# Kernel tuning notes

Hardware: AMD Instinct MI355X
Metric: run time of the kernel (lower is better)

The kernel has to match this reference:

```python
import jax, jax.numpy as jnp
import numpy as np

B, S, D, E, TOPK, H = 8, 2048, 2048, 8, 2, 16
DH = D // H          # head_dim = 128
FH = D // H          # head_hidden_dim = 128 (hidden == dim, forced by linear3 shapes)
ROUTE_LEN = 2048     # x0 = x[:, :2048]


def setup_inputs() -> dict:
    key = jax.random.key(0)
    ks = jax.random.split(key, 8)
    s = 0.02
    return {
        "x": jax.random.normal(ks[0], (B, S, D), jnp.float32),
        "switch_w": jax.random.normal(ks[1], (E, D * ROUTE_LEN), jnp.float32) * s,
        "switch_b": jnp.zeros((E,), jnp.float32),
        "w1": jax.random.normal(ks[2], (E, FH, DH), jnp.float32) * s,
        "b1": jnp.zeros((E, FH), jnp.float32),
        "w2": jax.random.normal(ks[3], (E, DH, FH), jnp.float32) * s,
        "b2": jnp.zeros((E, DH), jnp.float32),
        "w3": jax.random.normal(ks[4], (D, D), jnp.float32) * s,
        "b3": jnp.zeros((D,), jnp.float32),
    }


def reference(x, switch_w, switch_b, w1, b1, w2, b2, w3, b3):
    b, s, d = x.shape
    # --- router: per batch-sample softmax over experts, top-k selection ---
    x0 = x[:, :ROUTE_LEN].reshape(b, -1)                      # [B, 2048*D]
    logits = x0 @ switch_w.T + switch_b                       # [B, E]
    probs = jax.nn.softmax(logits, axis=-1)
    gate, top_idx = jax.lax.top_k(probs, TOPK)                # [B, K]
    # --- split heads ---
    xh = x.reshape(b, s, H, DH).transpose(0, 2, 1, 3)         # [B, H, S, Dh]
    # --- per-sample gather of selected expert weights (dense grouped GEMM) ---
    w1s, b1s = w1[top_idx], b1[top_idx]                       # [B,K,F,Dh], [B,K,F]
    w2s, b2s = w2[top_idx], b2[top_idx]                       # [B,K,Dh,F], [B,K,Dh]
    h = jnp.einsum('bhsd,bkfd->bkhsf', xh, w1s) + b1s[:, :, None, None, :]
    h = jax.nn.gelu(h, approximate=False)                     # torch nn.GELU is exact
    o = jnp.einsum('bkhsf,bkdf->bkhsd', h, w2s) + b2s[:, :, None, None, :]
    # gate-weighted combine over selected experts (index_add_ sums the k copies)
    o = (o * gate[:, :, None, None, None]).sum(axis=1)        # [B, H, S, Dh]
    o = o.transpose(0, 2, 1, 3).reshape(b, s, d)              # combine heads
    out = x + o                                               # residual
    return out @ w3.T + b3                                    # linear3
```

## Files before the change

kernel.cpp:

```cpp
#include <hip/hip_runtime.h>
#include <math.h>

typedef unsigned short u16;
typedef unsigned int u32;
typedef __attribute__((ext_vector_type(8))) short short8;
typedef __attribute__((ext_vector_type(4))) float f32x4;
typedef __attribute__((ext_vector_type(4))) unsigned short ushort4v;

#define B_ 8
#define S_ 2048
#define D_ 2048
#define H_ 16
#define RLEN 4194304
#define NCHUNK 512

static __device__ __forceinline__ u16 f2bf(float f) {
    union { float f; u32 u; } v; v.f = f;
    u32 r = v.u + 0x7fffu + ((v.u >> 16) & 1u);
    return (u16)(r >> 16);
}
static __device__ __forceinline__ float bf2f(u16 u) {
    union { u32 u; float f; } v; v.u = ((u32)u) << 16;
    return v.f;
}
static __device__ __forceinline__ float gelu_fast(float v) {
    float z = 1.5957691216057308f * v * (1.0f + 0.044715f * v * v);
    float e = __expf(z);
    float r = __builtin_amdgcn_rcpf(e + 1.0f);
    return v * (1.0f - r);
}
static __device__ __forceinline__ f32x4 ntload4(const float* p) {
    return __builtin_nontemporal_load((const f32x4*)p);
}

typedef const __attribute__((address_space(1))) u32* gas1_t;
typedef __attribute__((address_space(3))) u32* las3_t;
static __device__ __forceinline__ void gload_lds16(const void* g, void* l) {
    __builtin_amdgcn_global_load_lds((gas1_t)g, (las3_t)l, 16, 0, 0);
}

template<int XB>
__global__ __launch_bounds__(256, 3) void router_partial(const float* __restrict__ x,
                                                         const float* __restrict__ sw,
                                                         float* __restrict__ part,
                                                         u16* __restrict__ xb) {
    int c = blockIdx.x;
    int t = threadIdx.x;
    const int chunk = RLEN / NCHUNK;
    int base = c * chunk;
    float acc[8][8];
#pragma unroll
    for (int b = 0; b < 8; b++)
#pragma unroll
        for (int e = 0; e < 8; e++) acc[b][e] = 0.f;

    for (int it = 0; it < chunk / (256 * 4); ++it) {
        int i = base + (it * 256 + t) * 4;
        f32x4 xv[8];
#pragma unroll
        for (int b = 0; b < 8; b++) xv[b] = ntload4(&x[(size_t)b * RLEN + i]);
        if (XB) {
            int row = i >> 7, col = i & 127;
            int scol = (((col >> 3) ^ (row & 7)) << 3) | (col & 7);
#pragma unroll
            for (int b = 0; b < 8; b++) {
                ushort4v u;
                u.x = f2bf(xv[b].x); u.y = f2bf(xv[b].y);
                u.z = f2bf(xv[b].z); u.w = f2bf(xv[b].w);
                *(ushort4v*)&xb[(size_t)b * RLEN + (size_t)row * 128 + scol] = u;
            }
        }
        f32x4 sv = ntload4(&sw[i]);
#pragma unroll
        for (int e = 0; e < 8; e++) {
            f32x4 svn;
            if (e < 7) svn = ntload4(&sw[(size_t)(e + 1) * RLEN + i]);
#pragma unroll
            for (int b = 0; b < 8; b++)
                acc[b][e] += xv[b].x * sv.x + xv[b].y * sv.y +
                             xv[b].z * sv.z + xv[b].w * sv.w;
            sv = svn;
        }
    }

    __shared__ float red[4][64];
    int lane = t & 63, wv = t >> 6;
#pragma unroll
    for (int q = 0; q < 64; q++) {
        float v = acc[q >> 3][q & 7];
#pragma unroll
        for (int m = 32; m >= 1; m >>= 1) v += __shfl_xor(v, m, 64);
        if (lane == 0) red[wv][q] = v;
    }
    __syncthreads();
    if (t < 64) {
        float s = red[0][t] + red[1][t] + red[2][t] + red[3][t];
        part[(size_t)t * NCHUNK + c] = s;
    }
}

__global__ __launch_bounds__(128) void router_finish(const float* __restrict__ part,
                                                     const float* __restrict__ swb,
                                                     const float* __restrict__ b2,
                                                     float* __restrict__ gate,
                                                     int* __restrict__ idx,
                                                     float* __restrict__ bc) {
    int t = threadIdx.x;
    __shared__ float lg[64];
    __shared__ float sg[16];
    __shared__ int   si[16];
    if (t < 64) {
        float s = 0.f;
        for (int c = 0; c < NCHUNK; c++) s += part[(size_t)t * NCHUNK + c];
        lg[t] = s + swb[t & 7];
    }
    __syncthreads();
    if (t < 8) {
        int b = t;
        float m = -1e30f;
        for (int e = 0; e < 8; e++) m = fmaxf(m, lg[b * 8 + e]);
        float p[8]; float sum = 0.f;
        for (int e = 0; e < 8; e++) { p[e] = expf(lg[b * 8 + e] - m); sum += p[e]; }
        for (int e = 0; e < 8; e++) p[e] /= sum;
        int i1 = 0; float v1 = p[0];
        for (int e = 1; e < 8; e++) if (p[e] > v1) { v1 = p[e]; i1 = e; }
        int i2 = -1; float v2 = -1.f;
        for (int e = 0; e < 8; e++) if (e != i1 && p[e] > v2) { v2 = p[e]; i2 = e; }
        gate[b * 2 + 0] = v1; gate[b * 2 + 1] = v2;
        idx[b * 2 + 0] = i1;  idx[b * 2 + 1] = i2;
        sg[b * 2] = v1; sg[b * 2 + 1] = v2;
        si[b * 2] = i1; si[b * 2 + 1] = i2;
    }
    __syncthreads();
    for (int b = 0; b < 8; b++)
        bc[b * 128 + t] = sg[b * 2] * b2[si[b * 2] * 128 + t] +
                          sg[b * 2 + 1] * b2[si[b * 2 + 1] * 128 + t];
}

__global__ __launch_bounds__(256) void convert_w12(const float* __restrict__ w1,
                                                   const float* __restrict__ w2,
                                                   u16* __restrict__ w1b,
                                                   u16* __restrict__ w2b) {
    int i4 = (blockIdx.x * 256 + threadIdx.x) * 4;
    if (i4 < 131072) {
        int k = i4 & 127, f = (i4 >> 7) & 127;
        float4 v = *(const float4*)&w1[i4];
        int sc = ((((k >> 3) ^ (f & 7)) << 3) | (k & 7));
        ushort4v u;
        u.x = f2bf(v.x); u.y = f2bf(v.y); u.z = f2bf(v.z); u.w = f2bf(v.w);
        *(ushort4v*)&w1b[(i4 & ~127) + sc] = u;
    } else {
        int j = i4 - 131072;
        float4 v = *(const float4*)&w2[j];
        ushort4v u;
        u.x = f2bf(v.x); u.y = f2bf(v.y); u.z = f2bf(v.z); u.w = f2bf(v.w);
        *(ushort4v*)&w2b[j] = u;
    }
}

__global__ __launch_bounds__(256) void convert_w3(const float* __restrict__ w3,
                                                  u16* __restrict__ w3b) {
    size_t i = ((size_t)blockIdx.x * 256 + threadIdx.x) * 4;
    float4 v = *(const float4*)&w3[i];
    u16* d = &w3b[i];
    d[0] = f2bf(v.x); d[1] = f2bf(v.y); d[2] = f2bf(v.z); d[3] = f2bf(v.w);
}

template<int XB>
__global__ __launch_bounds__(512) void mlp_kernel(const void* __restrict__ xsrc_,
                                                  const u16* __restrict__ w1b,
                                                  const u16* __restrict__ w2b,
                                                  const float* __restrict__ b1,
                                                  const float* __restrict__ gate,
                                                  const int* __restrict__ idx,
                                                  const float* __restrict__ bc,
                                                  u16* __restrict__ y) {
    __shared__ __align__(16) u16 w1s[256 * 128];
    __shared__ __align__(16) u16 xs[2][64 * 128];
    __shared__ __align__(16) u16 hb[2][32 * 256];
    __shared__ __align__(16) u16 ob[2][32 * 128];
    const int t = threadIdx.x, lane = t & 63, w = t >> 6;
    const int wr = w >> 2, wq = w & 3;
    const int l15 = lane & 15, l4 = lane >> 4;
    const int b = blockIdx.y, grp = blockIdx.x;
    const size_t xbase = (size_t)b * RLEN;
    const size_t gbase = xbase + (size_t)grp * 65536;
    const int e0 = idx[b * 2], e1 = idx[b * 2 + 1];
    const int slot = wq >> 1;
    const float gw = gate[b * 2 + slot];
    const float* b1p = b1 + (slot ? e1 : e0) * 128;

    float b1v[4];
#pragma unroll
    for (int nt = 0; nt < 4; nt++) b1v[nt] = b1p[(wq & 1) * 64 + nt * 16 + l15];
    float bcv[2];
#pragma unroll
    for (int n = 0; n < 2; n++) bcv[n] = bc[b * 128 + wq * 32 + n * 16 + l15];

    short8 w2f[2][8];
#pragma unroll
    for (int n = 0; n < 2; n++) {
        int d = wq * 32 + n * 16 + l15;
#pragma unroll
        for (int kb = 0; kb < 8; kb++) {
            int e = (kb >= 4) ? e1 : e0;
            int f = (kb & 3) * 32 + l4 * 8;
            w2f[n][kb] = *(const short8*)&w2b[((size_t)(e * 128 + d)) * 128 + f];
        }
    }

#pragma unroll
    for (int p = 0; p < 8; p++) {
        int elem = p * 4096 + t * 8;
        int frow = elem >> 7, col = elem & 127;
        int e = (frow >= 128) ? e1 : e0;
        gload_lds16(w1b + ((size_t)(e * 128 + (frow & 127))) * 128 + col,
                    (char*)w1s + elem * 2);
    }
    if (XB) {
        const u16* xbp = (const u16*)xsrc_;
#pragma unroll
        for (int T = 0; T < 2; T++) {
            gload_lds16(xbp + gbase + T * 8192 + t * 8, (char*)&xs[T][0] + t * 16);
            gload_lds16(xbp + gbase + T * 8192 + 4096 + t * 8,
                        (char*)&xs[T][0] + 8192 + t * 16);
        }
        asm volatile("s_waitcnt vmcnt(0)" ::: "memory");
    } else {
        const float* xf = (const float*)xsrc_;
#pragma unroll
        for (int T = 0; T < 2; T++)
#pragma unroll
            for (int p = 0; p < 4; p++) {
                int elem = p * 2048 + t * 4;
                int row = elem >> 7, col = elem & 127;
                float4 v = *(const float4*)&xf[gbase + T * 8192 + elem];
                ushort4v u;
                u.x = f2bf(v.x); u.y = f2bf(v.y); u.z = f2bf(v.z); u.w = f2bf(v.w);
                *(ushort4v*)((char*)&xs[T][0] + row * 256 +
                             (((col >> 3) ^ (row & 7)) << 4) + (col & 7) * 2) = u;
            }
        asm volatile("s_waitcnt vmcnt(0) lgkmcnt(0)" ::: "memory");
    }
    __builtin_amdgcn_s_barrier();

    auto G1 = [&](int st, f32x4* a1) {
        const u16* xc = &xs[(st >> 1) & 1][0];
        int rbase = (st & 1) * 32 + wr * 16 + l15;
#pragma unroll
        for (int nt = 0; nt < 4; nt++) a1[nt] = (f32x4){0.f, 0.f, 0.f, 0.f};
#pragma unroll
        for (int kb = 0; kb < 4; kb++) {
            int kg = kb * 4 + l4;
            short8 a = *(const short8*)&xc[rbase * 128 + ((kg ^ (rbase & 7)) << 3)];
#pragma unroll
            for (int nt = 0; nt < 4; nt++) {
                int fr = wq * 64 + nt * 16 + l15;
                short8 bb = *(const short8*)&w1s[fr * 128 + ((kg ^ (fr & 7)) << 3)];
                a1[nt] = __builtin_amdgcn_mfma_f32_16x16x32_bf16(a, bb, a1[nt], 0, 0, 0);
            }
        }
    };
    auto GELU_ST = [&](int st, f32x4* a1) {
        u16* hd = &hb[st & 1][0];
#pragma unroll
        for (int nt = 0; nt < 4; nt++) {
            int fcol = wq * 64 + nt * 16 + l15;
#pragma unroll
            for (int j = 0; j < 4; j++) {
                int row = wr * 16 + l4 * 4 + j;
                float v = a1[nt][j] + b1v[nt];
                v = gelu_fast(v) * gw;
                hd[row * 256 + ((((fcol >> 3) ^ (row & 7)) << 3) | (fcol & 7))] = f2bf(v);
            }
        }
    };
    auto G2 = [&](int st, f32x4* a2) {
        const u16* hs = &hb[st & 1][0];
        int arow = wr * 16 + l15;
        a2[0] = (f32x4){0.f, 0.f, 0.f, 0.f};
        a2[1] = (f32x4){0.f, 0.f, 0.f, 0.f};
#pragma unroll
        for (int kb = 0; kb < 8; kb++) {
            int fg = kb * 4 + l4;
            short8 a = *(const short8*)&hs[arow * 256 + ((fg ^ (arow & 7)) << 3)];
            a2[0] = __builtin_amdgcn_mfma_f32_16x16x32_bf16(a, w2f[0][kb], a2[0], 0, 0, 0);
            a2[1] = __builtin_amdgcn_mfma_f32_16x16x32_bf16(a, w2f[1][kb], a2[1], 0, 0, 0);
        }
    };
    auto OWRITE = [&](int st, f32x4* a2) {
        u16* od = &ob[st & 1][0];
        const u16* xc = &xs[(st >> 1) & 1][0];
#pragma unroll
        for (int n = 0; n < 2; n++) {
            int d = wq * 32 + n * 16 + l15;
#pragma unroll
            for (int j = 0; j < 4; j++) {
                int row = wr * 16 + l4 * 4 + j;
                int xrow = (st & 1) * 32 + row;
                float xr = bf2f(xc[xrow * 128 + ((((d >> 3) ^ (xrow & 7)) << 3) | (d & 7))]);
                od[row * 128 + (d ^ ((row & 7) << 3))] = f2bf(a2[n][j] + bcv[n] + xr);
            }
        }
    };
    auto YSTV = [&](int st) {
        int row = t >> 4;
        int cg = t & 15;
        const u16* os = &ob[st & 1][0];
        short8 v = *(const short8*)&os[row * 128 + ((cg ^ (row & 7)) << 3)];
        u16* yb = y + xbase + (size_t)grp * 65536 + st * 4096;
        *(short8*)&yb[row * 128 + cg * 8] = v;
    };

    {
        f32x4 a1[4];
        G1(0, a1);
        GELU_ST(0, a1);
    }
    asm volatile("s_waitcnt lgkmcnt(0)" ::: "memory");
    __builtin_amdgcn_s_barrier();

    for (int st = 0; st < 17; ++st) {
        const bool stg = (st < 16) && ((st & 1) == 0) && st >= 2 && st <= 12;
        if (st < 16) {
            f32x4 a1n[4];
            if (st < 15) G1(st + 1, a1n);
            f32x4 a2[2];
            G2(st, a2);
            if (st < 15) GELU_ST(st + 1, a1n);
            OWRITE(st, a2);
        }
        if (stg) {
            int T = st / 2 + 1;
            if (XB) {
                const u16* xbp = (const u16*)xsrc_;
                gload_lds16(xbp + gbase + T * 8192 + t * 8, (char*)&xs[T & 1][0] + t * 16);
                gload_lds16(xbp + gbase + T * 8192 + 4096 + t * 8,
                            (char*)&xs[T & 1][0] + 8192 + t * 16);
            } else {
                const float* xf = (const float*)xsrc_;
#pragma unroll
                for (int p = 0; p < 4; p++) {
                    int elem = p * 2048 + t * 4;
                    int row = elem >> 7, col = elem & 127;
                    float4 v = *(const float4*)&xf[gbase + T * 8192 + elem];
                    ushort4v u;
                    u.x = f2bf(v.x); u.y = f2bf(v.y); u.z = f2bf(v.z); u.w = f2bf(v.w);
                    *(ushort4v*)((char*)&xs[T & 1][0] + row * 256 +
                                 (((col >> 3) ^ (row & 7)) << 4) + (col & 7) * 2) = u;
                }
            }
        }
        if (st >= 1) YSTV(st - 1);
        asm volatile("s_waitcnt lgkmcnt(0)" ::: "memory");
        if (stg && XB) asm volatile("s_waitcnt vmcnt(1)" ::: "memory");
        if (st < 16) __builtin_amdgcn_s_barrier();
    }
}

#define BARX() do { asm volatile("" ::: "memory"); __builtin_amdgcn_s_barrier(); \
                    asm volatile("" ::: "memory"); } while (0)

#define WLG(NSTR) do { asm volatile("s_waitcnt lgkmcnt(" NSTR ")" ::: "memory"); \
                       __builtin_amdgcn_sched_barrier(0); } while (0)

#define DSA(mh, c) do { \
    const char* _ba = smem + (c) * 65536 + abase; \
    _Pragma("unroll") for (int mf = 0; mf < 4; mf++) \
    _Pragma("unroll") for (int kk = 0; kk < 2; kk++) \
        areg[mf][kk] = *(const short8*)(_ba + ((mh) * 4 + mf) * 2048 + kof[kk]); \
} while (0)

#define DSB(nh, c) do { \
    const char* _bb = smem + (c) * 65536 + bbase; \
    _Pragma("unroll") for (int nf = 0; nf < 2; nf++) \
    _Pragma("unroll") for (int kk = 0; kk < 2; kk++) \
        breg[(nh) * 2 + nf][kk] = *(const short8*)(_bb + ((nh) * 2 + nf) * 2048 + kof[kk]); \
} while (0)

#define MMAQ(mh, nh) do { \
    __builtin_amdgcn_s_setprio(1); \
    _Pragma("unroll") for (int mf = 0; mf < 4; mf++) \
    _Pragma("unroll") for (int nf = 0; nf < 2; nf++) \
    _Pragma("unroll") for (int kk = 0; kk < 2; kk++) \
        acc[(mh) * 4 + mf][(nh) * 2 + nf] = __builtin_amdgcn_mfma_f32_16x16x32_bf16( \
            areg[mf][kk], breg[(nh) * 2 + nf][kk], acc[(mh) * 4 + mf][(nh) * 2 + nf], 0, 0, 0); \
    __builtin_amdgcn_s_setprio(0); \
} while (0)

#define STG(op, c, h, kt) do { \
    const u16* _gs = (op) ? wbp : yap; \
    int _tr0 = (op) ? nrow0 : mrow0; \
    _Pragma("unroll") for (int p = 0; p < 2; p++) { \
        int _idx = p * 512 + t; \
        int _row = _idx >> 3; \
        int _gcol = (((_idx & 7) ^ (_row & 7)) << 3); \
        gload_lds16(_gs + (size_t)(_tr0 + (h) * 128 + _row) * 2048 + (kt) * 64 + _gcol, \
                    smem + (c) * 65536 + (op) * 32768 + (h) * 16384 + _idx * 16); \
    } \
} while (0)

__global__ __launch_bounds__(512, 2) void final_gemm256(const u16* __restrict__ yap,
                                                        const u16* __restrict__ wbp,
                                                        const float* __restrict__ b3,
                                                        float* __restrict__ out) {
    extern __shared__ char smem[];
    const int t = threadIdx.x;
    const int lane = t & 63, w = t >> 6;
    const int wm = w >> 2, wn = w & 3;
    const int l15 = lane & 15, l4 = lane >> 4, sx = lane & 7;

    int bid = blockIdx.x;
    int swz = (bid & 7) * 64 + (bid >> 3);
    int nblk = swz >> 6, mblk = swz & 63;
    const int mrow0 = mblk * 256;
    const int nrow0 = nblk * 256;

    const int abase = wm * 16384 + l15 * 128;
    const int bbase = 32768 + (wn >> 1) * 16384 + ((wn & 1) * 64 + l15) * 128;
    int kof[2];
#pragma unroll
    for (int kk = 0; kk < 2; kk++) kof[kk] = ((kk * 4 + l4) ^ sx) << 4;

    f32x4 acc[8][4];
#pragma unroll
    for (int m = 0; m < 8; m++)
#pragma unroll
        for (int n = 0; n < 4; n++) acc[m][n] = (f32x4){0.f, 0.f, 0.f, 0.f};
    short8 areg[4][2];
    short8 breg[4][2];

    STG(0, 0, 0, 0); STG(0, 0, 1, 0); STG(1, 0, 0, 0); STG(1, 0, 1, 0);
    STG(0, 1, 0, 1); STG(0, 1, 1, 1); STG(1, 1, 0, 1); STG(1, 1, 1, 1);
    asm volatile("s_waitcnt vmcnt(8)" ::: "memory");
    BARX();
    DSA(0, 0); DSB(0, 0); DSB(1, 0);

    for (int it2 = 0; it2 < 16; ++it2) {
#pragma unroll
        for (int c = 0; c < 2; ++c) {
            const int tt = 2 * it2 + c;
            WLG("4");  MMAQ(0, 0);
            WLG("0");  MMAQ(0, 1);
            DSA(1, c);
            WLG("0");  MMAQ(1, 0);
            asm volatile("s_waitcnt vmcnt(0)" ::: "memory");
            BARX();
            if (tt < 30) { STG(0, c, 0, tt + 2); STG(0, c, 1, tt + 2);
                           STG(1, c, 0, tt + 2); STG(1, c, 1, tt + 2); }
            MMAQ(1, 1);
            if (tt < 31) { DSA(0, c ^ 1); DSB(0, c ^ 1); DSB(1, c ^ 1); }
        }
    }

#pragma unroll
    for (int m = 0; m < 8; m++)
#pragma unroll
        for (int n = 0; n < 4; n++) {
            int col = nrow0 + wn * 64 + n * 16 + l15;
            float bias = b3[col];
            int row = mrow0 + wm * 128 + m * 16 + l4 * 4;
#pragma unroll
            for (int j = 0; j < 4; j++)
                __builtin_nontemporal_store(acc[m][n][j] + bias,
                                            &out[(size_t)(row + j) * 2048 + col]);
        }
}

extern "C" void kernel_launch(void* const* d_in, const int* in_sizes, int n_in,
                              void* d_out, int out_size, void* d_ws, size_t ws_size,
                              hipStream_t stream) {
    const float* x   = (const float*)d_in[0];
    const float* sw  = (const float*)d_in[1];
    const float* swb = (const float*)d_in[2];
    const float* w1  = (const float*)d_in[3];
    const float* b1  = (const float*)d_in[4];
    const float* w2  = (const float*)d_in[5];
    const float* b2  = (const float*)d_in[6];
    const float* w3  = (const float*)d_in[7];
    const float* b3  = (const float*)d_in[8];
    float* out = (float*)d_out;

    char* ws = (char*)d_ws;
    float* part = (float*)(ws + 0);
    float* gate = (float*)(ws + 131072);
    int*   idx  = (int*)(ws + 131136);
    float* bc   = (float*)(ws + 131200);
    u16*   w1b  = (u16*)(ws + 262144);
    u16*   w2b  = (u16*)(ws + 524288);
    u16*   w3b  = (u16*)(ws + 786432);
    u16*   y    = (u16*)(ws + 9175040);
    u16*   xb   = (u16*)(ws + 76283904);
    const size_t need_xb = 143392768;
    const bool xbmode = ws_size >= need_xb;

    hipFuncSetAttribute((const void*)final_gemm256,
                        hipFuncAttributeMaxDynamicSharedMemorySize, 131072);

    if (xbmode)
        hipLaunchKernelGGL((router_partial<1>), dim3(NCHUNK), dim3(256), 0, stream, x, sw, part, xb);
    else
        hipLaunchKernelGGL((router_partial<0>), dim3(NCHUNK), dim3(256), 0, stream, x, sw, part, xb);
    hipLaunchKernelGGL(router_finish, dim3(1), dim3(128), 0, stream, part, swb, b2, gate, idx, bc);
    hipLaunchKernelGGL(convert_w12, dim3(256), dim3(256), 0, stream, w1, w2, w1b, w2b);
    hipLaunchKernelGGL(convert_w3, dim3(D_ * D_ / 1024), dim3(256), 0, stream, w3, w3b);
    if (xbmode)
        hipLaunchKernelGGL((mlp_kernel<1>), dim3(64, 8), dim3(512), 0, stream,
                           (const void*)xb, w1b, w2b, b1, gate, idx, bc, y);
    else
        hipLaunchKernelGGL((mlp_kernel<0>), dim3(64, 8), dim3(512), 0, stream,
                           (const void*)x, w1b, w2b, b1, gate, idx, bc, y);
    hipLaunchKernelGGL(final_gemm256, dim3(512), dim3(512), 131072, stream,
                       y, w3b, b3, out);
}
```

Before: 313.6 us.

## Restructure linear3 GEMM main loop into finer-grained interleaved load/MFMA schedule

Rewrites the bf16 output GEMM's K loop so that global-to-LDS staging loads are issued one quarter-tile at a time between MFMA quadrants, with barriers around each MFMA group and explicit vmcnt/lgkmcnt waits. It replaces the old schedule, which waited for all global loads and issued four staging loads at once, and adds an explicit epilogue for the last tiles. The goal is to spread memory traffic across compute and keep waves in lockstep, at the cost of many more barriers. The output stores also switch from nontemporal to regular stores.

```diff
diff --git a/kernel.cpp b/kernel.cpp
--- a/kernel.cpp
+++ b/kernel.cpp
@@ -360,9 +360,10 @@
 
 #define BARX() do { asm volatile("" ::: "memory"); __builtin_amdgcn_s_barrier(); \
                     asm volatile("" ::: "memory"); } while (0)
-
-#define WLG(NSTR) do { asm volatile("s_waitcnt lgkmcnt(" NSTR ")" ::: "memory"); \
-                       __builtin_amdgcn_sched_barrier(0); } while (0)
+#define WLGC(NSTR) do { asm volatile("s_waitcnt lgkmcnt(" NSTR ")" ::: "memory"); \
+                        __builtin_amdgcn_sched_barrier(0); } while (0)
+#define WVMC(NSTR) do { asm volatile("s_waitcnt vmcnt(" NSTR ")" ::: "memory"); \
+                        __builtin_amdgcn_sched_barrier(0); } while (0)
 
 #define DSA(mh, c) do { \
     const char* _ba = smem + (c) * 65536 + abase; \
@@ -430,27 +431,45 @@
     short8 areg[4][2];
     short8 breg[4][2];
 
-    STG(0, 0, 0, 0); STG(0, 0, 1, 0); STG(1, 0, 0, 0); STG(1, 0, 1, 0);
-    STG(0, 1, 0, 1); STG(0, 1, 1, 1); STG(1, 1, 0, 1); STG(1, 1, 1, 1);
-    asm volatile("s_waitcnt vmcnt(8)" ::: "memory");
+    STG(1, 0, 0, 0); STG(1, 0, 1, 0); STG(0, 0, 0, 0); STG(0, 0, 1, 0);
+    STG(1, 1, 0, 1); STG(1, 1, 1, 1);
+    WVMC("4");
     BARX();
-    DSA(0, 0); DSB(0, 0); DSB(1, 0);
-
-    for (int it2 = 0; it2 < 16; ++it2) {
-#pragma unroll
-        for (int c = 0; c < 2; ++c) {
-            const int tt = 2 * it2 + c;
-            WLG("4");  MMAQ(0, 0);
-            WLG("0");  MMAQ(0, 1);
-            DSA(1, c);
-            WLG("0");  MMAQ(1, 0);
-            asm volatile("s_waitcnt vmcnt(0)" ::: "memory");
-            BARX();
-            if (tt < 30) { STG(0, c, 0, tt + 2); STG(0, c, 1, tt + 2);
-                           STG(1, c, 0, tt + 2); STG(1, c, 1, tt + 2); }
-            MMAQ(1, 1);
-            if (tt < 31) { DSA(0, c ^ 1); DSB(0, c ^ 1); DSB(1, c ^ 1); }
-        }
+
+    for (int i = 0; i < 15; ++i) {
+        const int to = 2 * i + 1, te2 = 2 * i + 2, to2 = 2 * i + 3;
+        DSA(0, 0); DSB(0, 0); STG(0, 1, 0, to);
+        WLGC("8"); BARX(); WLGC("0"); MMAQ(0, 0); BARX();
+        DSB(1, 0); STG(0, 1, 1, to);
+        BARX(); WLGC("0"); MMAQ(0, 1); BARX();
+        DSA(1, 0); STG(1, 0, 0, te2);
+        BARX(); WLGC("0"); MMAQ(1, 0); BARX();
+        STG(1, 0, 1, te2);
+        WVMC("4"); BARX(); MMAQ(1, 1); BARX();
+        DSA(0, 1); DSB(0, 1); STG(0, 0, 0, te2);
+        WLGC("8"); BARX(); WLGC("0"); MMAQ(0, 0); BARX();
+        DSB(1, 1); STG(0, 0, 1, te2);
+        BARX(); WLGC("0"); MMAQ(0, 1); BARX();
+        DSA(1, 1); STG(1, 1, 0, to2);
+        BARX(); WLGC("0"); MMAQ(1, 0); BARX();
+        STG(1, 1, 1, to2);
+        WVMC("4"); BARX(); MMAQ(1, 1); BARX();
+    }
+    {
+        DSA(0, 0); DSB(0, 0); STG(0, 1, 0, 31);
+        WLGC("8"); BARX(); WLGC("0"); MMAQ(0, 0); BARX();
+        DSB(1, 0); STG(0, 1, 1, 31);
+        BARX(); WLGC("0"); MMAQ(0, 1); BARX();
+        DSA(1, 0);
+        BARX(); WLGC("0"); MMAQ(1, 0); BARX();
+        WVMC("0"); BARX(); MMAQ(1, 1); BARX();
+        DSA(0, 1); DSB(0, 1);
+        WLGC("8"); BARX(); WLGC("0"); MMAQ(0, 0); BARX();
+        DSB(1, 1);
+        BARX(); WLGC("0"); MMAQ(0, 1); BARX();
+        DSA(1, 1);
+        BARX(); WLGC("0"); MMAQ(1, 0); BARX();
+        MMAQ(1, 1);
     }
 
 #pragma unroll
@@ -462,8 +481,7 @@
             int row = mrow0 + wm * 128 + m * 16 + l4 * 4;
 #pragma unroll
             for (int j = 0; j < 4; j++)
-                __builtin_nontemporal_store(acc[m][n][j] + bias,
-                                            &out[(size_t)(row + j) * 2048 + col]);
+                out[(size_t)(row + j) * 2048 + col] = acc[m][n][j] + bias;
         }
 }
 
```

New measurement: 312.0 us. About the same (-0.5%).
